# Kernel tuning notes

Hardware: AMD Instinct MI355X
Metric: run time of the kernel (lower is better)

The kernel has to match this reference:

```python
import jax, jax.numpy as jnp
import numpy as np

FRAME_PERIOD = 80   # samples per frame
IR_LENGTH = 2000    # filter length L (taps = L-1)
N_FFT = 4096


def setup_inputs() -> dict:
    key = jax.random.key(0)
    k1, k2 = jax.random.split(key)
    x = jax.random.normal(k1, (2, 24000), dtype=jnp.float32)          # waveform, T = 300*80
    mc = jax.random.normal(k2, (2, 300, 25), dtype=jnp.float32) * 0.1  # mel-cepstrum (B, N, M+1)
    return {"x": x, "mc": mc}


def _c2min_phase_ir(c):
    # cepstrum -> minimum-phase impulse response: ifft(exp(fft(c))) truncated.
    # (alpha=0, gamma=0 makes mgc2ir exactly this FFT-based conversion.)
    C = jnp.fft.fft(c, n=N_FFT, axis=-1)
    h = jnp.fft.ifft(jnp.exp(C), axis=-1).real[..., :IR_LENGTH]
    return h


def _linear_interpolate(h):
    # (B, N, L) frame-rate filters -> (B, N*P, L) sample-rate filters,
    # linear interpolation between consecutive frames, last frame replicated.
    B, N, L = h.shape
    P = FRAME_PERIOD
    h_next = jnp.concatenate([h[:, 1:], h[:, -1:]], axis=1)
    w = (jnp.arange(P, dtype=h.dtype) / P)[None, None, :, None]  # (1,1,P,1)
    y = h[:, :, None, :] * (1.0 - w) + h_next[:, :, None, :] * w  # (B,N,P,L)
    return y.reshape(B, N * P, L)


def reference(x, mc):
    L = IR_LENGTH
    h = _c2min_phase_ir(mc)      # (B, N, L) minimum-phase IR
    h = jnp.flip(h, axis=-1)     # phase == 'minimum': flip taps
    h = _linear_interpolate(h)   # (B, T, L)
    T = h.shape[1]
    # causal padding (taps, 0) then unfold into overlapping windows
    x_pad = jnp.pad(x, ((0, 0), (L - 1, 0)))
    idx = jnp.arange(T)[:, None] + jnp.arange(L)[None, :]  # (T, L)
    windows = x_pad[:, idx]                                # (B, T, L)
    y = jnp.sum(windows * h, axis=-1)                      # (B, T)
    return y
```

## Files before the change

kernel.cpp:

```cpp
#include <hip/hip_runtime.h>
#include <math.h>

#define IR_LEN  2000
#define PFRAME  80
#define NFRAMES 300
#define NBATCH  2
#define NROWS   (NBATCH*NFRAMES)
#define T_TOTAL (NFRAMES*PFRAME)
#define NCOEF   25
#define TWO_PI  6.283185307179586f
#define GS      68
#define XWN     2160
#define XWPAD   2432

#define XPHYS(B) ((B) + (((B) >> 5) << 2))

__device__ __forceinline__ void fsincos(float a, float* s, float* c) {
    *s = __sinf(a); *c = __cosf(a);
}

__global__ __launch_bounds__(256) void minphase_fir_fused(
        const float* __restrict__ mc, const float* __restrict__ x,
        float* __restrict__ y) {
    __shared__ __align__(16) float U[8704];
    __shared__ __align__(16) float xws[XWPAD];
    __shared__ float csh[NCOEF];
    float* const EHr = U;
    float* const EHi = U + 4096;
    float* const Gr  = U;
    float* const Gi  = U + 4352;
    float* const hU  = U;
    float* const red = U + 4224;

    const int row   = blockIdx.x;
    const int batch = row / NFRAMES;
    const int frame = row - batch * NFRAMES;
    const int t0    = frame * PFRAME;
    const int t     = threadIdx.x;

    if (t < NCOEF) csh[t] = mc[row * NCOEF + t];

    float xv[9];
    {
        const float* xb = x + batch * T_TOTAL;
        #pragma unroll
        for (int k = 0; k < 9; k++) {
            const int j  = t + 256 * k;
            const int xi = t0 - 2079 + j;
            xv[k] = (j < XWN && xi >= 0 && xi < T_TOTAL) ? xb[xi] : 0.0f;
        }
    }

    {
        const int rph = blockIdx.x >> 8;
        if (rph == 1)      asm volatile("s_sleep 32");
        else if (rph == 2) asm volatile("s_sleep 64");
    }
    __syncthreads();

    {
        float creg[NCOEF];
        #pragma unroll
        for (int k = 0; k < NCOEF; k++) creg[k] = csh[k];

        float bs, bc; fsincos(-(TWO_PI / 4096.0f) * (float)t, &bs, &bc);
        const float SC =  0.923879532511287f;
        const float SS = -0.382683432365090f;
        #pragma unroll 4
        for (int ii = 0; ii < 8; ii++) {
            const int f = t + 256 * ii;
            const float wc = bc, ws = bs;
            { const float nr = bc * SC - bs * SS;
              const float ni = bc * SS + bs * SC;
              bc = nr; bs = ni; }
            const float t2 = 2.0f * wc;
            float b1 = 0.0f, b2 = 0.0f;
            #pragma unroll
            for (int k = NCOEF - 1; k >= 1; k--) {
                const float bk = __fmaf_rn(t2, b1, creg[k] - b2);
                b2 = b1; b1 = bk;
            }
            const float Cr = __fmaf_rn(wc, b1, creg[0] - b2);
            const float Ci = ws * b1;
            const float m = __expf(Cr);
            float si, co; fsincos(Ci, &si, &co);
            const float er = m * co, ei = m * si;
            EHr[f] = er; EHi[f] = ei;
            if (f > 0) { EHr[4096 - f] = er; EHi[4096 - f] = -ei; }
        }
        if (t == 0) {
            float Cr = 0.0f, Ci = 0.0f;
            float cr = 1.0f, ci = 0.0f;
            #pragma unroll
            for (int k = 0; k < NCOEF; k++) {
                Cr += csh[k] * cr; Ci += csh[k] * ci;
                cr = -cr; ci = -ci;
            }
            const float m = __expf(Cr);
            float si, co; fsincos(Ci, &si, &co);
            EHr[2048] = m * co; EHi[2048] = m * si;
        }
    }

    #pragma unroll
    for (int k = 0; k < 9; k++) {
        const int j = t + 256 * k;
        if (j < XWN) xws[XPHYS(j)] = xv[k];
    }
    __syncthreads();

    {
        const bool act = t < 144;
        const int bg = t % 9;
        const int dp = t / 9;
        const int b0 = bg * 4;
        const int d0 = dp * 2;
        float Ter[2][4], Tei[2][4], Tor[2][4], Toi[2][4];
        #pragma unroll
        for (int j = 0; j < 2; j++)
            #pragma unroll
            for (int i = 0; i < 4; i++) {
                Ter[j][i] = 0.0f; Tei[j][i] = 0.0f;
                Tor[j][i] = 0.0f; Toi[j][i] = 0.0f;
            }
        float rr[2], ri[2], wr[2], wi[2];
        if (act) {
            #pragma unroll
            for (int j = 0; j < 2; j++) {
                float s, c; fsincos((TWO_PI / 32.0f) * (float)(d0 + j), &s, &c);
                wr[j] = c; wi[j] = s; rr[j] = 1.0f; ri[j] = 0.0f;
            }
            float4 vre = *(const float4*)&EHr[b0];
            float4 vie = *(const float4*)&EHi[b0];
            float4 vro = *(const float4*)&EHr[64 + b0];
            float4 vio = *(const float4*)&EHi[64 + b0];
            #pragma unroll 4
            for (int a2 = 0; a2 < 32; a2++) {
                const float4 cre = vre, cie = vie, cro = vro, cio = vio;
                if (a2 < 31) {
                    const int nb = 128 * (a2 + 1) + b0;
                    vre = *(const float4*)&EHr[nb];
                    vie = *(const float4*)&EHi[nb];
                    vro = *(const float4*)&EHr[nb + 64];
                    vio = *(const float4*)&EHi[nb + 64];
                }
                const float ere[4] = {cre.x, cre.y, cre.z, cre.w};
                const float eie[4] = {cie.x, cie.y, cie.z, cie.w};
                const float ero[4] = {cro.x, cro.y, cro.z, cro.w};
                const float eio[4] = {cio.x, cio.y, cio.z, cio.w};
                #pragma unroll
                for (int j = 0; j < 2; j++) {
                    #pragma unroll
                    for (int i = 0; i < 4; i++) {
                        Ter[j][i] += ere[i] * rr[j] - eie[i] * ri[j];
                        Tei[j][i] += ere[i] * ri[j] + eie[i] * rr[j];
                        Tor[j][i] += ero[i] * rr[j] - eio[i] * ri[j];
                        Toi[j][i] += ero[i] * ri[j] + eio[i] * rr[j];
                    }
                    const float nr = rr[j] * wr[j] - ri[j] * wi[j];
                    const float ni = rr[j] * wi[j] + ri[j] * wr[j];
                    rr[j] = nr; ri[j] = ni;
                }
            }
        }
        __syncthreads();

        if (act) {
            float os[2], oc[2];
            #pragma unroll
            for (int j = 0; j < 2; j++)
                fsincos((TWO_PI / 64.0f) * (float)(d0 + j), &os[j], &oc[j]);
            #pragma unroll
            for (int i = 0; i < 4; i++) {
                const int b = b0 + i;
                if (b > 32) continue;
                float gpr[2], gpi[2], gmr[2], gmi[2];
                #pragma unroll
                for (int j = 0; j < 2; j++) {
                    const int d = d0 + j;
                    const float ur = oc[j] * Tor[j][i] - os[j] * Toi[j][i];
                    const float ui = oc[j] * Toi[j][i] + os[j] * Tor[j][i];
                    const float pr = Ter[j][i] + ur, pi = Tei[j][i] + ui;
                    const float mr = Ter[j][i] - ur, mi = Tei[j][i] - ui;
                    float s, c;
                    fsincos((TWO_PI / 4096.0f) * (float)(b * d), &s, &c);
                    gpr[j] = pr * c - pi * s; gpi[j] = pr * s + pi * c;
                    fsincos((TWO_PI / 4096.0f) * (float)(b * (d + 32)), &s, &c);
                    gmr[j] = mr * c - mi * s; gmi[j] = mr * s + mi * c;
                }
                *(float2*)&Gr[b * GS + d0]      = make_float2(gpr[0], gpr[1]);
                *(float2*)&Gi[b * GS + d0]      = make_float2(gpi[0], gpi[1]);
                *(float2*)&Gr[b * GS + d0 + 32] = make_float2(gmr[0], gmr[1]);
                *(float2*)&Gi[b * GS + d0 + 32] = make_float2(gmi[0], gmi[1]);
            }
        }
    }
    __syncthreads();

    float hv[4][2];
    int   dl_, cg_;
    {
        const int dl = (t & 31) * 2;
        const int cg = t >> 5;
        dl_ = dl; cg_ = cg;
        float swi_, swr_; fsincos((TWO_PI / 64.0f) * (float)cg, &swi_, &swr_);
        const float swr = swr_, swi = swi_;
        float rr = 1.0f, ri = 0.0f;
        float acc00 = 0, acc01 = 0, acc10 = 0, acc11 = 0;
        float acc20 = 0, acc21 = 0, acc30 = 0, acc31 = 0;
        int bb = 0;

#define S2C 0.70710678118654752f
#define STEP2(f8r, f8i, f16r, f16i, f24r, f24i)                                \
        {                                                                      \
            const float2 g_r = *(const float2*)&Gr[bb * GS + dl];              \
            const float2 g_i = *(const float2*)&Gi[bb * GS + dl];              \
            acc00 += g_r.x * rr - g_i.x * ri;                                  \
            acc01 += g_r.y * rr - g_i.y * ri;                                  \
            { const float tr = rr*(f8r) - ri*(f8i), ti = rr*(f8i) + ri*(f8r);  \
              acc10 += g_r.x * tr - g_i.x * ti;                                \
              acc11 += g_r.y * tr - g_i.y * ti; }                              \
            { const float tr = rr*(f16r) - ri*(f16i), ti = rr*(f16i) + ri*(f16r); \
              acc20 += g_r.x * tr - g_i.x * ti;                                \
              acc21 += g_r.y * tr - g_i.y * ti; }                              \
            { const float tr = rr*(f24r) - ri*(f24i), ti = rr*(f24i) + ri*(f24r); \
              acc30 += g_r.x * tr - g_i.x * ti;                                \
              acc31 += g_r.y * tr - g_i.y * ti; }                              \
            { const float nr = rr * swr - ri * swi;                            \
              const float ni = rr * swi + ri * swr;                            \
              rr = nr; ri = ni; }                                              \
            bb++;                                                              \
        }

        #pragma unroll 1
        for (int grp = 0; grp < 4; grp++) {
            STEP2( 1.0f, 0.0f,   1.0f, 0.0f,   1.0f, 0.0f)
            STEP2( S2C,  S2C,    0.0f, 1.0f,  -S2C,  S2C)
            STEP2( 0.0f, 1.0f,  -1.0f, 0.0f,   0.0f,-1.0f)
            STEP2(-S2C,  S2C,    0.0f,-1.0f,   S2C,  S2C)
            STEP2(-1.0f, 0.0f,   1.0f, 0.0f,  -1.0f, 0.0f)
            STEP2(-S2C, -S2C,    0.0f, 1.0f,   S2C, -S2C)
            STEP2( 0.0f,-1.0f,  -1.0f, 0.0f,   0.0f, 1.0f)
            STEP2( S2C, -S2C,    0.0f,-1.0f,  -S2C, -S2C)
        }
#undef STEP2

        const float g0a  = Gr[dl],           g0b  = Gr[dl + 1];
        const float g32a = Gr[32 * GS + dl], g32b = Gr[32 * GS + dl + 1];
        const float sgn  = (cg & 1) ? -1.0f : 1.0f;
        const float sc = 1.0f / 4096.0f;
        hv[0][0] = (2.0f * acc00 - g0a + sgn * g32a) * sc;
        hv[0][1] = (2.0f * acc01 - g0b + sgn * g32b) * sc;
        hv[1][0] = (2.0f * acc10 - g0a + sgn * g32a) * sc;
        hv[1][1] = (2.0f * acc11 - g0b + sgn * g32b) * sc;
        hv[2][0] = (2.0f * acc20 - g0a + sgn * g32a) * sc;
        hv[2][1] = (2.0f * acc21 - g0b + sgn * g32b) * sc;
        hv[3][0] = (2.0f * acc30 - g0a + sgn * g32a) * sc;
        hv[3][1] = (2.0f * acc31 - g0b + sgn * g32b) * sc;
    }
    __syncthreads();

    #pragma unroll
    for (int v = 0; v < 4; v++) {
        const int c = cg_ + 8 * v;
        const int n = 64 * c + dl_;
        if (n < IR_LEN)     hU[n]     = hv[v][0];
        if (n + 1 < IR_LEN) hU[n + 1] = hv[v][1];
    }
    __syncthreads();

    if (t < 240) {
        const int o0 = (t % 20) * 8;
        const int kc = t / 20;
        const int kb = kc * 168;
        const int ns = (kc == 11) ? 38 : 42;
        float s0[8] = {0,0,0,0,0,0,0,0};
        int Bo = o0 + 1996 - kb;
        float4 w1 = *(const float4*)&xws[XPHYS(Bo + 4)];
        float4 w2 = *(const float4*)&xws[XPHYS(Bo + 8)];
        for (int s = 0; s < ns; s++) {
            const float4 w0 = *(const float4*)&xws[XPHYS(Bo)];
            const float4 ha = *(const float4*)&hU[kb + 4 * s];
            const float wv[12] = {w0.x, w0.y, w0.z, w0.w,
                                  w1.x, w1.y, w1.z, w1.w,
                                  w2.x, w2.y, w2.z, w2.w};
            const float hav[4] = {ha.x, ha.y, ha.z, ha.w};
            #pragma unroll
            for (int jo = 0; jo < 8; jo++) {
                #pragma unroll
                for (int jk = 0; jk < 4; jk++) {
                    s0[jo] += hav[jk] * wv[3 + jo - jk];
                }
            }
            w2 = w1; w1 = w0; Bo -= 4;
        }
        const int rb = kc * 168 + o0;
        *(float4*)&red[rb]     = make_float4(s0[0], s0[1], s0[2], s0[3]);
        *(float4*)&red[rb + 4] = make_float4(s0[4], s0[5], s0[6], s0[7]);
    }
    __syncthreads();

    if (t < 160) {
        float z = 0.0f;
        #pragma unroll
        for (int kc = 0; kc < 12; kc++) z += red[kc * 168 + t];
        const int o = t;
        const int tout = t0 - PFRAME + o;
        float wgt = (o < PFRAME) ? (float)o * (1.0f / PFRAME)
                                 : (float)(160 - o) * (1.0f / PFRAME);
        if (frame == NFRAMES - 1 && o >= PFRAME) wgt = 1.0f;
        if (tout >= 0) {
            atomicAdd(&y[batch * T_TOTAL + tout], wgt * z);
        }
    }
}

extern "C" void kernel_launch(void* const* d_in, const int* in_sizes, int n_in,
                              void* d_out, int out_size, void* d_ws, size_t ws_size,
                              hipStream_t stream) {
    const float* x  = (const float*)d_in[0];
    const float* mc = (const float*)d_in[1];
    float* y = (float*)d_out;

    hipMemsetAsync(y, 0, (size_t)out_size * sizeof(float), stream);
    minphase_fir_fused<<<NROWS, 256, 0, stream>>>(mc, x, y);
}
```

Baseline: 86.60 us.

## Compact spectrum storage and add radix-4 pre-stage to shrink inverse DFT work

```diff
diff --git a/kernel.cpp b/kernel.cpp
--- a/kernel.cpp
+++ b/kernel.cpp
@@ -22,15 +22,19 @@
 __global__ __launch_bounds__(256) void minphase_fir_fused(
         const float* __restrict__ mc, const float* __restrict__ x,
         float* __restrict__ y) {
-    __shared__ __align__(16) float U[8704];
+    __shared__ __align__(16) float SH[9216];
     __shared__ __align__(16) float xws[XWPAD];
     __shared__ float csh[NCOEF];
-    float* const EHr = U;
-    float* const EHi = U + 4096;
-    float* const Gr  = U;
-    float* const Gi  = U + 4352;
-    float* const hU  = U;
-    float* const red = U + 4224;
+    float* const Ecr = SH;
+    float* const Eci = SH + 2304;
+    float* const Per = SH + 4608;
+    float* const Pei = SH + 5760;
+    float* const Por = SH + 6912;
+    float* const Poi = SH + 8064;
+    float* const Gr  = SH;
+    float* const Gi  = SH + 2304;
+    float* const hU  = SH;
+    float* const red = SH + 4608;
 
     const int row   = blockIdx.x;
     const int batch = row / NFRAMES;
@@ -62,6 +66,13 @@
         float creg[NCOEF];
         #pragma unroll
         for (int k = 0; k < NCOEF; k++) creg[k] = csh[k];
+
+        const int  m   = t & 127;
+        const bool lD  = (m < 36) || (m >= 64 && m < 100);
+        const int  cbD = (m < 64) ? m : m - 28;
+        const int  mm  = (128 - m) & 127;
+        const bool lM  = (mm < 36) || (mm >= 64 && mm < 100);
+        const int  cbM = (mm < 64) ? mm : mm - 28;
 
         float bs, bc; fsincos(-(TWO_PI / 4096.0f) * (float)t, &bs, &bc);
         const float SC =  0.923879532511287f;
@@ -82,11 +93,15 @@
             }
             const float Cr = __fmaf_rn(wc, b1, creg[0] - b2);
             const float Ci = ws * b1;
-            const float m = __expf(Cr);
+            const float mg = __expf(Cr);
             float si, co; fsincos(Ci, &si, &co);
-            const float er = m * co, ei = m * si;
-            EHr[f] = er; EHi[f] = ei;
-            if (f > 0) { EHr[4096 - f] = er; EHi[4096 - f] = -ei; }
+            const float er = mg * co, ei = mg * si;
+            const int aD = (t >> 7) + 2 * ii;
+            if (lD) { Ecr[72 * aD + cbD] = er; Eci[72 * aD + cbD] = ei; }
+            if (f > 0 && lM) {
+                const int aM = (m == 0) ? (32 - aD) : (31 - aD);
+                Ecr[72 * aM + cbM] = er; Eci[72 * aM + cbM] = -ei;
+            }
         }
         if (t == 0) {
             float Cr = 0.0f, Ci = 0.0f;
@@ -96,9 +111,9 @@
                 Cr += csh[k] * cr; Ci += csh[k] * ci;
                 cr = -cr; ci = -ci;
             }
-            const float m = __expf(Cr);
+            const float mg = __expf(Cr);
             float si, co; fsincos(Ci, &si, &co);
-            EHr[2048] = m * co; EHi[2048] = m * si;
+            Ecr[72 * 16] = mg * co; Eci[72 * 16] = mg * si;
         }
     }
 
@@ -106,6 +121,61 @@
     for (int k = 0; k < 9; k++) {
         const int j = t + 256 * k;
         if (j < XWN) xws[XPHYS(j)] = xv[k];
+    }
+    __syncthreads();
+
+    if (t < 144) {
+        const int bg = t % 9;
+        const int rh = t / 9;
+        const int r  = rh & 7;
+        const int h  = rh >> 3;
+        const int base = 72 * r + 36 * h + 4 * bg;
+        float e0r[4], e1r[4], e2r[4], e3r[4];
+        float e0i[4], e1i[4], e2i[4], e3i[4];
+        {
+            const float4 a = *(const float4*)&Ecr[base];
+            const float4 b = *(const float4*)&Ecr[base + 576];
+            const float4 c = *(const float4*)&Ecr[base + 1152];
+            const float4 d = *(const float4*)&Ecr[base + 1728];
+            e0r[0]=a.x; e0r[1]=a.y; e0r[2]=a.z; e0r[3]=a.w;
+            e1r[0]=b.x; e1r[1]=b.y; e1r[2]=b.z; e1r[3]=b.w;
+            e2r[0]=c.x; e2r[1]=c.y; e2r[2]=c.z; e2r[3]=c.w;
+            e3r[0]=d.x; e3r[1]=d.y; e3r[2]=d.z; e3r[3]=d.w;
+        }
+        {
+            const float4 a = *(const float4*)&Eci[base];
+            const float4 b = *(const float4*)&Eci[base + 576];
+            const float4 c = *(const float4*)&Eci[base + 1152];
+            const float4 d = *(const float4*)&Eci[base + 1728];
+            e0i[0]=a.x; e0i[1]=a.y; e0i[2]=a.z; e0i[3]=a.w;
+            e1i[0]=b.x; e1i[1]=b.y; e1i[2]=b.z; e1i[3]=b.w;
+            e2i[0]=c.x; e2i[1]=c.y; e2i[2]=c.z; e2i[3]=c.w;
+            e3i[0]=d.x; e3i[1]=d.y; e3i[2]=d.z; e3i[3]=d.w;
+        }
+        float p0r[4], p0i[4], p1r[4], p1i[4];
+        float p2r[4], p2i[4], p3r[4], p3i[4];
+        #pragma unroll
+        for (int i = 0; i < 4; i++) {
+            const float Ar = e0r[i] + e2r[i], Ai = e0i[i] + e2i[i];
+            const float Br = e0r[i] - e2r[i], Bi = e0i[i] - e2i[i];
+            const float Cr = e1r[i] + e3r[i], Ci = e1i[i] + e3i[i];
+            const float Dr = e1r[i] - e3r[i], Di = e1i[i] - e3i[i];
+            p0r[i] = Ar + Cr;  p0i[i] = Ai + Ci;
+            p2r[i] = Ar - Cr;  p2i[i] = Ai - Ci;
+            p1r[i] = Br - Di;  p1i[i] = Bi + Dr;
+            p3r[i] = Br + Di;  p3i[i] = Bi - Dr;
+        }
+        float* const Qr = (h ? Por : Per);
+        float* const Qi = (h ? Poi : Pei);
+        const int pb = 144 * r + 4 * bg;
+        *(float4*)&Qr[pb]       = make_float4(p0r[0], p0r[1], p0r[2], p0r[3]);
+        *(float4*)&Qi[pb]       = make_float4(p0i[0], p0i[1], p0i[2], p0i[3]);
+        *(float4*)&Qr[pb + 36]  = make_float4(p1r[0], p1r[1], p1r[2], p1r[3]);
+        *(float4*)&Qi[pb + 36]  = make_float4(p1i[0], p1i[1], p1i[2], p1i[3]);
+        *(float4*)&Qr[pb + 72]  = make_float4(p2r[0], p2r[1], p2r[2], p2r[3]);
+        *(float4*)&Qi[pb + 72]  = make_float4(p2i[0], p2i[1], p2i[2], p2i[3]);
+        *(float4*)&Qr[pb + 108] = make_float4(p3r[0], p3r[1], p3r[2], p3r[3]);
+        *(float4*)&Qi[pb + 108] = make_float4(p3i[0], p3i[1], p3i[2], p3i[3]);
     }
     __syncthreads();
 
@@ -123,49 +193,37 @@
                 Ter[j][i] = 0.0f; Tei[j][i] = 0.0f;
                 Tor[j][i] = 0.0f; Toi[j][i] = 0.0f;
             }
-        float rr[2], ri[2], wr[2], wi[2];
         if (act) {
             #pragma unroll
             for (int j = 0; j < 2; j++) {
-                float s, c; fsincos((TWO_PI / 32.0f) * (float)(d0 + j), &s, &c);
-                wr[j] = c; wi[j] = s; rr[j] = 1.0f; ri[j] = 0.0f;
-            }
-            float4 vre = *(const float4*)&EHr[b0];
-            float4 vie = *(const float4*)&EHi[b0];
-            float4 vro = *(const float4*)&EHr[64 + b0];
-            float4 vio = *(const float4*)&EHi[64 + b0];
-            #pragma unroll 4
-            for (int a2 = 0; a2 < 32; a2++) {
-                const float4 cre = vre, cie = vie, cro = vro, cio = vio;
-                if (a2 < 31) {
-                    const int nb = 128 * (a2 + 1) + b0;
-                    vre = *(const float4*)&EHr[nb];
-                    vie = *(const float4*)&EHi[nb];
-                    vro = *(const float4*)&EHr[nb + 64];
-                    vio = *(const float4*)&EHi[nb + 64];
-                }
-                const float ere[4] = {cre.x, cre.y, cre.z, cre.w};
-                const float eie[4] = {cie.x, cie.y, cie.z, cie.w};
-                const float ero[4] = {cro.x, cro.y, cro.z, cro.w};
-                const float eio[4] = {cio.x, cio.y, cio.z, cio.w};
+                const int d  = d0 + j;
+                const int pb = 36 * (d & 3) + b0;
+                float s, c; fsincos((TWO_PI / 32.0f) * (float)d, &s, &c);
+                const float wr = c, wi = s;
+                float rr = 1.0f, ri = 0.0f;
                 #pragma unroll
-                for (int j = 0; j < 2; j++) {
+                for (int r8 = 0; r8 < 8; r8++) {
+                    const int pa = 144 * r8 + pb;
+                    const float4 vpr = *(const float4*)&Per[pa];
+                    const float4 vpi = *(const float4*)&Pei[pa];
+                    const float4 vqr = *(const float4*)&Por[pa];
+                    const float4 vqi = *(const float4*)&Poi[pa];
+                    const float per_[4] = {vpr.x, vpr.y, vpr.z, vpr.w};
+                    const float pei_[4] = {vpi.x, vpi.y, vpi.z, vpi.w};
+                    const float por_[4] = {vqr.x, vqr.y, vqr.z, vqr.w};
+                    const float poi_[4] = {vqi.x, vqi.y, vqi.z, vqi.w};
                     #pragma unroll
                     for (int i = 0; i < 4; i++) {
-                        Ter[j][i] += ere[i] * rr[j] - eie[i] * ri[j];
-                        Tei[j][i] += ere[i] * ri[j] + eie[i] * rr[j];
-                        Tor[j][i] += ero[i] * rr[j] - eio[i] * ri[j];
-                        Toi[j][i] += ero[i] * ri[j] + eio[i] * rr[j];
+                        Ter[j][i] += per_[i] * rr - pei_[i] * ri;
+                        Tei[j][i] += per_[i] * ri + pei_[i] * rr;
+                        Tor[j][i] += por_[i] * rr - poi_[i] * ri;
+                        Toi[j][i] += por_[i] * ri + poi_[i] * rr;
                     }
-                    const float nr = rr[j] * wr[j] - ri[j] * wi[j];
-                    const float ni = rr[j] * wi[j] + ri[j] * wr[j];
-                    rr[j] = nr; ri[j] = ni;
+                    const float nr = rr * wr - ri * wi;
+                    const float ni = rr * wi + ri * wr;
+                    rr = nr; ri = ni;
                 }
             }
-        }
-        __syncthreads();
-
-        if (act) {
             float os[2], oc[2];
             #pragma unroll
             for (int j = 0; j < 2; j++)
```

New measurement: 94.98 us. +9.7%, slower.
